# Kernel tuning notes

Measured on AMD Instinct MI355X. Metric: run time of the kernel, lower is better.

The kernel has to match this reference:

```python
import jax, jax.numpy as jnp
import numpy as np

EPS = 1e-5
MIN_NORM = 1e-15


def artanh(x):
    return jnp.arctanh(jnp.clip(x, -1.0 + EPS, 1.0 - EPS))


def expmap0(u, c):
    # Poincare ball exponential map at the origin (HGCN style)
    sqrt_c = jnp.sqrt(c)
    u_norm = jnp.maximum(jnp.linalg.norm(u, axis=-1, keepdims=True), MIN_NORM)
    return jnp.tanh(sqrt_c * u_norm) * u / (sqrt_c * u_norm)


def mobius_add(x, y, c):
    x2 = jnp.sum(x * x, axis=-1, keepdims=True)
    y2 = jnp.sum(y * y, axis=-1, keepdims=True)
    xy = jnp.sum(x * y, axis=-1, keepdims=True)
    num = (1.0 + 2.0 * c * xy + c * y2) * x + (1.0 - c * x2) * y
    den = 1.0 + 2.0 * c * xy + (c ** 2) * x2 * y2
    return num / jnp.maximum(den, MIN_NORM)


def sqdist(x, y, c):
    sqrt_c = jnp.sqrt(c)
    ma = mobius_add(-x, y, c)
    dist = (2.0 / sqrt_c) * artanh(sqrt_c * jnp.linalg.norm(ma, axis=-1))
    return dist ** 2


def setup_inputs() -> dict:
    key = jax.random.key(0)
    k1, k2 = jax.random.split(key)
    B, T, N, C, K = 8, 12, 325, 32, 100
    # scale down so points land well inside the unit ball (curvature c=1)
    node_repr = 0.05 * jax.random.normal(k1, (B, T, N, C), dtype=jnp.float32)
    centroid_weight = 0.05 * jax.random.normal(k2, (K, C), dtype=jnp.float32)
    c = jnp.ones((1,), dtype=jnp.float32)
    return {"node_repr": node_repr, "centroid_weight": centroid_weight, "c": c}


def reference(node_repr, centroid_weight, c):
    cc = c[0]
    B, T, N, C = node_repr.shape
    # centroid embedding lookup of arange(K) == the weight table itself
    centroids = expmap0(centroid_weight, cc)          # [K, C]
    x = node_repr[..., None, :]                        # [B, T, N, 1, C]
    node_centroid_dist = sqdist(x, centroids, cc)      # [B, T, N, K] via broadcast
    graph_centroid_dist = jnp.sum(node_centroid_dist, axis=1) / N  # [B, N, K] (faithful to dim=1 in source)
    return graph_centroid_dist, node_centroid_dist
```

## Files before the change

kernel.cpp:

```cpp
#include <hip/hip_runtime.h>

namespace {
constexpr int B = 8, T = 12, N = 325, C = 32, K = 100;
constexpr int KPAD = 36;
constexpr int NPB = 2;
constexpr int NPAIRS = (N + NPB - 1) / NPB;
constexpr float EPSF = 1e-5f;
constexpr float MIN_NORM = 1e-15f;
}

__global__ __launch_bounds__(256) void hcd_kernel(
    const float* __restrict__ x_g,
    const float* __restrict__ cw,
    const float* __restrict__ cptr,
    float* __restrict__ out0,
    float* __restrict__ out1)
{
  __shared__ float yl[K][KPAD];
  __shared__ float y2l[K];
  __shared__ float x2l[NPB][T];

  const int tid = threadIdx.x;
  const int b  = blockIdx.x / NPAIRS;
  const int np = blockIdx.x % NPAIRS;
  const int n0 = np * NPB;
  const float c  = cptr[0];
  const float sc = sqrtf(c);
  const float inv_c4 = 4.f / c;
  const float HLN2 = 0.34657359028f;
  const float TLOG2E = 2.88539008178f;

  if (tid < K) {
    float u[C];
    float u2 = 0.f;
    #pragma unroll
    for (int q = 0; q < C / 4; ++q) {
      float4 v = *(const float4*)(cw + tid * C + 4 * q);
      u[4*q+0] = v.x; u[4*q+1] = v.y; u[4*q+2] = v.z; u[4*q+3] = v.w;
    }
    #pragma unroll
    for (int i = 0; i < C; ++i) u2 = fmaf(u[i], u[i], u2);
    float z = sc * fmaxf(sqrtf(u2), MIN_NORM);
    float E  = exp2f(z * TLOG2E);
    float th = (E - 1.f) * __builtin_amdgcn_rcpf(E + 1.f);
    float f  = th * __builtin_amdgcn_rcpf(z);
    #pragma unroll
    for (int q = 0; q < C / 4; ++q) {
      float4 v = make_float4(f*u[4*q+0], f*u[4*q+1], f*u[4*q+2], f*u[4*q+3]);
      *(float4*)&yl[tid][4 * q] = v;
    }
    y2l[tid] = f * f * u2;
  }

  if (tid >= 128 && tid < 128 + NPB * T) {
    int i  = tid - 128;
    int nl = i / T, t = i - nl * T;
    int n  = n0 + nl;
    if (n < N) {
      const float* xr = x_g + ((size_t)(b * T + t) * N + n) * C;
      float s = 0.f;
      #pragma unroll
      for (int q = 0; q < C / 4; ++q) {
        float4 v = *(const float4*)(xr + 4 * q);
        s = fmaf(v.x, v.x, s); s = fmaf(v.y, v.y, s);
        s = fmaf(v.z, v.z, s); s = fmaf(v.w, v.w, s);
      }
      x2l[nl][t] = s;
    }
  }
  __syncthreads();

  const int grp = tid >> 7;
  const int k   = tid & 127;
  const int n   = n0 + grp;
  if (n < N) {
    const int kc = (k < K) ? k : (K - 1);

    float yk[C];
    #pragma unroll
    for (int q = 0; q < C / 4; ++q) {
      float4 v = *(const float4*)&yl[kc][4 * q];
      yk[4*q+0] = v.x; yk[4*q+1] = v.y; yk[4*q+2] = v.z; yk[4*q+3] = v.w;
    }
    const float y2 = y2l[kc];
    const float c2 = c * c;
    const float tc = 2.f * c;

    int rowbase = ((b * T) * N + n) * C;
    rowbase = __builtin_amdgcn_readfirstlane(rowbase);

    float ssum = 0.f;
    #pragma unroll
    for (int t = 0; t < T; ++t) {
      const float* xr = x_g + rowbase + t * (N * C);
      float a0 = 0.f, a1 = 0.f, a2 = 0.f, a3 = 0.f;
      #pragma unroll
      for (int j = 0; j < C; j += 4) {
        a0 = fmaf(xr[j+0], yk[j+0], a0);
        a1 = fmaf(xr[j+1], yk[j+1], a1);
        a2 = fmaf(xr[j+2], yk[j+2], a2);
        a3 = fmaf(xr[j+3], yk[j+3], a3);
      }
      const float dot = (a0 + a1) + (a2 + a3);

      const float x2 = x2l[grp][t];
      const float xy = -dot;
      const float A  = fmaf(tc, xy, 1.f) + c * y2;
      const float Bc = 1.f - c * x2;
      float num2 = A * A * x2 + Bc * Bc * y2 + 2.f * A * Bc * xy;
      num2 = fmaxf(num2, 0.f);
      float den = fmaf(c2 * x2, y2, fmaf(tc, xy, 1.f));
      den = fmaxf(den, MIN_NORM);
      float s_ = sc * __builtin_amdgcn_sqrtf(num2);
      s_ = fminf(s_, (1.f - EPSF) * den);
      float r  = (den + s_) * __builtin_amdgcn_rcpf(den - s_);
      float at = HLN2 * __builtin_amdgcn_logf(r);
      float d2 = inv_c4 * at * at;
      ssum += d2;
      if (k < K)
        out1[(((size_t)(b * T + t)) * N + n) * K + k] = d2;
    }
    if (k < K)
      out0[((size_t)b * N + n) * K + k] = ssum * (1.f / (float)N);
  }
}

extern "C" void kernel_launch(void* const* d_in, const int* in_sizes, int n_in,
                              void* d_out, int out_size, void* d_ws, size_t ws_size,
                              hipStream_t stream) {
  const void* xp = nullptr; const void* cwp = nullptr; const void* cp = nullptr;
  for (int i = 0; i < n_in; ++i) {
    if (in_sizes[i] == B * T * N * C)      xp  = d_in[i];
    else if (in_sizes[i] == K * C)         cwp = d_in[i];
    else if (in_sizes[i] == 1)             cp  = d_in[i];
  }
  if (!xp)  xp  = d_in[0];
  if (!cwp) cwp = d_in[1];
  if (!cp)  cp  = d_in[n_in - 1];

  float* out0 = (float*)d_out;
  float* out1 = out0 + (size_t)B * N * K;

  hipLaunchKernelGGL(hcd_kernel, dim3(B * NPAIRS), dim3(256), 0, stream,
                     (const float*)xp, (const float*)cwp, (const float*)cp,
                     out0, out1);
}
```

Baseline: 18.65 us.

## Use 5 nodes per block, per-thread centroid expmap, scalar-load x rows

Each block now handles 5 nodes with 640 threads (two waves per node) instead of 2 nodes with 256 threads, which cuts the number of blocks. The shared-memory centroid table is removed: each thread loads its centroid row from global memory and recomputes the expmap scaling itself. The per-timestep x row is read through inline-asm s_load_dwordx16 scalar loads with an explicit wait, replacing the compiler's per-element loads. In exchange, the expmap work is repeated across waves, each load waits fully before compute so there is no overlap, and the x2 setup no longer bounds-checks n, which relies on N being divisible by 5.

```diff
diff --git a/kernel.cpp b/kernel.cpp
--- a/kernel.cpp
+++ b/kernel.cpp
@@ -2,22 +2,21 @@
 
 namespace {
 constexpr int B = 8, T = 12, N = 325, C = 32, K = 100;
-constexpr int KPAD = 36;
-constexpr int NPB = 2;
-constexpr int NPAIRS = (N + NPB - 1) / NPB;
+constexpr int NPB = 5;
+constexpr int NPAIRS = N / NPB;
 constexpr float EPSF = 1e-5f;
 constexpr float MIN_NORM = 1e-15f;
 }
 
-__global__ __launch_bounds__(256) void hcd_kernel(
+typedef float f32x16 __attribute__((ext_vector_type(16)));
+
+__global__ __launch_bounds__(640) void hcd_kernel(
     const float* __restrict__ x_g,
     const float* __restrict__ cw,
     const float* __restrict__ cptr,
     float* __restrict__ out0,
     float* __restrict__ out1)
 {
-  __shared__ float yl[K][KPAD];
-  __shared__ float y2l[K];
   __shared__ float x2l[NPB][T];
 
   const int tid = threadIdx.x;
@@ -30,99 +29,105 @@
   const float HLN2 = 0.34657359028f;
   const float TLOG2E = 2.88539008178f;
 
-  if (tid < K) {
-    float u[C];
+  if (tid < NPB * T) {
+    int nl_ = tid / T, t = tid - nl_ * T;
+    const float* xr = x_g + ((size_t)(b * T + t) * N + (n0 + nl_)) * C;
+    float s = 0.f;
+    #pragma unroll
+    for (int q = 0; q < C / 4; ++q) {
+      float4 v = *(const float4*)(xr + 4 * q);
+      s = fmaf(v.x, v.x, s); s = fmaf(v.y, v.y, s);
+      s = fmaf(v.z, v.z, s); s = fmaf(v.w, v.w, s);
+    }
+    x2l[nl_][t] = s;
+  }
+
+  const int wave = tid >> 6;
+  const int lane = tid & 63;
+  const int nl = wave >> 1;
+  const int h  = wave & 1;
+  const int k  = h * 64 + lane;
+  const int kc = (k < K) ? k : K - 1;
+  const bool pred = (k < K);
+
+  float yk[C];
+  float y2;
+  {
+    const float* yr = cw + kc * C;
+    #pragma unroll
+    for (int q = 0; q < C / 4; ++q) {
+      float4 v = *(const float4*)(yr + 4 * q);
+      yk[4*q+0] = v.x; yk[4*q+1] = v.y; yk[4*q+2] = v.z; yk[4*q+3] = v.w;
+    }
     float u2 = 0.f;
     #pragma unroll
-    for (int q = 0; q < C / 4; ++q) {
-      float4 v = *(const float4*)(cw + tid * C + 4 * q);
-      u[4*q+0] = v.x; u[4*q+1] = v.y; u[4*q+2] = v.z; u[4*q+3] = v.w;
-    }
-    #pragma unroll
-    for (int i = 0; i < C; ++i) u2 = fmaf(u[i], u[i], u2);
+    for (int i = 0; i < C; ++i) u2 = fmaf(yk[i], yk[i], u2);
     float z = sc * fmaxf(sqrtf(u2), MIN_NORM);
     float E  = exp2f(z * TLOG2E);
     float th = (E - 1.f) * __builtin_amdgcn_rcpf(E + 1.f);
     float f  = th * __builtin_amdgcn_rcpf(z);
     #pragma unroll
-    for (int q = 0; q < C / 4; ++q) {
-      float4 v = make_float4(f*u[4*q+0], f*u[4*q+1], f*u[4*q+2], f*u[4*q+3]);
-      *(float4*)&yl[tid][4 * q] = v;
-    }
-    y2l[tid] = f * f * u2;
-  }
-
-  if (tid >= 128 && tid < 128 + NPB * T) {
-    int i  = tid - 128;
-    int nl = i / T, t = i - nl * T;
-    int n  = n0 + nl;
-    if (n < N) {
-      const float* xr = x_g + ((size_t)(b * T + t) * N + n) * C;
-      float s = 0.f;
-      #pragma unroll
-      for (int q = 0; q < C / 4; ++q) {
-        float4 v = *(const float4*)(xr + 4 * q);
-        s = fmaf(v.x, v.x, s); s = fmaf(v.y, v.y, s);
-        s = fmaf(v.z, v.z, s); s = fmaf(v.w, v.w, s);
-      }
-      x2l[nl][t] = s;
-    }
+    for (int i = 0; i < C; ++i) yk[i] *= f;
+    y2 = f * f * u2;
   }
   __syncthreads();
 
-  const int grp = tid >> 7;
-  const int k   = tid & 127;
-  const int n   = n0 + grp;
-  if (n < N) {
-    const int kc = (k < K) ? k : (K - 1);
+  const int n = n0 + nl;
+  int rowbase = ((b * T) * N + n) * C;
+  rowbase = __builtin_amdgcn_readfirstlane(rowbase);
+  const float* xbase = x_g + rowbase;
 
-    float yk[C];
+  const float c2 = c * c;
+  const float tc = 2.f * c;
+  float ssum = 0.f;
+
+  #pragma unroll
+  for (int t = 0; t < T; ++t) {
+    const float* xt = xbase + t * (N * C);
+    f32x16 xa, xv;
+    asm volatile(
+        "s_load_dwordx16 %0, %2, 0x0\n\t"
+        "s_load_dwordx16 %1, %2, 0x40\n\t"
+        "s_waitcnt lgkmcnt(0)"
+        : "=&s"(xa), "=&s"(xv)
+        : "s"(xt));
+
+    float a0 = 0.f, a1 = 0.f, a2 = 0.f, a3 = 0.f;
     #pragma unroll
-    for (int q = 0; q < C / 4; ++q) {
-      float4 v = *(const float4*)&yl[kc][4 * q];
-      yk[4*q+0] = v.x; yk[4*q+1] = v.y; yk[4*q+2] = v.z; yk[4*q+3] = v.w;
+    for (int i = 0; i < 16; i += 4) {
+      a0 = fmaf(xa[i+0], yk[i+0], a0);
+      a1 = fmaf(xa[i+1], yk[i+1], a1);
+      a2 = fmaf(xa[i+2], yk[i+2], a2);
+      a3 = fmaf(xa[i+3], yk[i+3], a3);
     }
-    const float y2 = y2l[kc];
-    const float c2 = c * c;
-    const float tc = 2.f * c;
+    #pragma unroll
+    for (int i = 0; i < 16; i += 4) {
+      a0 = fmaf(xv[i+0], yk[16+i+0], a0);
+      a1 = fmaf(xv[i+1], yk[16+i+1], a1);
+      a2 = fmaf(xv[i+2], yk[16+i+2], a2);
+      a3 = fmaf(xv[i+3], yk[16+i+3], a3);
+    }
+    const float dot = (a0 + a1) + (a2 + a3);
 
-    int rowbase = ((b * T) * N + n) * C;
-    rowbase = __builtin_amdgcn_readfirstlane(rowbase);
-
-    float ssum = 0.f;
-    #pragma unroll
-    for (int t = 0; t < T; ++t) {
-      const float* xr = x_g + rowbase + t * (N * C);
-      float a0 = 0.f, a1 = 0.f, a2 = 0.f, a3 = 0.f;
-      #pragma unroll
-      for (int j = 0; j < C; j += 4) {
-        a0 = fmaf(xr[j+0], yk[j+0], a0);
-        a1 = fmaf(xr[j+1], yk[j+1], a1);
-        a2 = fmaf(xr[j+2], yk[j+2], a2);
-        a3 = fmaf(xr[j+3], yk[j+3], a3);
-      }
-      const float dot = (a0 + a1) + (a2 + a3);
-
-      const float x2 = x2l[grp][t];
-      const float xy = -dot;
-      const float A  = fmaf(tc, xy, 1.f) + c * y2;
-      const float Bc = 1.f - c * x2;
-      float num2 = A * A * x2 + Bc * Bc * y2 + 2.f * A * Bc * xy;
-      num2 = fmaxf(num2, 0.f);
-      float den = fmaf(c2 * x2, y2, fmaf(tc, xy, 1.f));
-      den = fmaxf(den, MIN_NORM);
-      float s_ = sc * __builtin_amdgcn_sqrtf(num2);
-      s_ = fminf(s_, (1.f - EPSF) * den);
-      float r  = (den + s_) * __builtin_amdgcn_rcpf(den - s_);
-      float at = HLN2 * __builtin_amdgcn_logf(r);
-      float d2 = inv_c4 * at * at;
-      ssum += d2;
-      if (k < K)
-        out1[(((size_t)(b * T + t)) * N + n) * K + k] = d2;
-    }
-    if (k < K)
-      out0[((size_t)b * N + n) * K + k] = ssum * (1.f / (float)N);
+    const float x2 = x2l[nl][t];
+    const float xy = -dot;
+    const float A  = fmaf(tc, xy, 1.f) + c * y2;
+    const float Bc = 1.f - c * x2;
+    float num2 = A * A * x2 + Bc * Bc * y2 + 2.f * A * Bc * xy;
+    num2 = fmaxf(num2, 0.f);
+    float den = fmaf(c2 * x2, y2, fmaf(tc, xy, 1.f));
+    den = fmaxf(den, MIN_NORM);
+    float s_ = sc * __builtin_amdgcn_sqrtf(num2);
+    s_ = fminf(s_, (1.f - EPSF) * den);
+    float r  = (den + s_) * __builtin_amdgcn_rcpf(den - s_);
+    float at = HLN2 * __builtin_amdgcn_logf(r);
+    float d2 = inv_c4 * at * at;
+    ssum += d2;
+    if (pred)
+      out1[(((size_t)(b * T + t)) * N + n) * K + k] = d2;
   }
+  if (pred)
+    out0[((size_t)b * N + n) * K + k] = ssum * (1.f / (float)N);
 }
 
 extern "C" void kernel_launch(void* const* d_in, const int* in_sizes, int n_in,
@@ -141,7 +146,7 @@
   float* out0 = (float*)d_out;
   float* out1 = out0 + (size_t)B * N * K;
 
-  hipLaunchKernelGGL(hcd_kernel, dim3(B * NPAIRS), dim3(256), 0, stream,
+  hipLaunchKernelGGL(hcd_kernel, dim3(B * NPAIRS), dim3(640), 0, stream,
                      (const float*)xp, (const float*)cwp, (const float*)cp,
                      out0, out1);
 }
```

Result: slower. 22.35 us (+19.9%).

## Compute node-centroid dot products with split-bf16 MFMA, five nodes per block

Applied to the files above, without the earlier changes.

Replaces the scalar per-thread 32-element FMA dot products with MFMA 16x16x32 bf16 instructions. Each fp32 operand is split into a high and a low bf16 part and three MFMAs are issued to keep close to fp32 accuracy. Each block now processes five nodes, one wave per node, with time steps mapped to MFMA rows and centroids to columns. The graph sum is reduced with cross-lane shuffles. This cuts VALU work and redundant global reads of x, at the cost of padding waste (T=12 padded to 16, K=100 padded to 112) and a small precision loss from dropping the low×low term.

```diff
diff --git a/kernel.cpp b/kernel.cpp
--- a/kernel.cpp
+++ b/kernel.cpp
@@ -2,22 +2,36 @@
 
 namespace {
 constexpr int B = 8, T = 12, N = 325, C = 32, K = 100;
-constexpr int KPAD = 36;
-constexpr int NPB = 2;
-constexpr int NPAIRS = (N + NPB - 1) / NPB;
+constexpr int NPB = 5;
+constexpr int NPAIRS = N / NPB;
+constexpr int KT = 7;
+constexpr int KP = KT * 16;
 constexpr float EPSF = 1e-5f;
 constexpr float MIN_NORM = 1e-15f;
 }
 
-__global__ __launch_bounds__(256) void hcd_kernel(
+typedef __attribute__((ext_vector_type(8))) short bf16x8;
+typedef __attribute__((ext_vector_type(4))) float f32x4;
+
+__device__ __forceinline__ unsigned short bf16_rne(float x) {
+  unsigned int u = __float_as_uint(x);
+  unsigned int r = u + 0x7FFFu + ((u >> 16) & 1u);
+  return (unsigned short)(r >> 16);
+}
+__device__ __forceinline__ float bf16_f(unsigned short h) {
+  return __uint_as_float(((unsigned int)h) << 16);
+}
+
+__global__ __launch_bounds__(320) void hcd_kernel(
     const float* __restrict__ x_g,
     const float* __restrict__ cw,
     const float* __restrict__ cptr,
     float* __restrict__ out0,
     float* __restrict__ out1)
 {
-  __shared__ float yl[K][KPAD];
-  __shared__ float y2l[K];
+  __shared__ unsigned short yh[KP][C];
+  __shared__ unsigned short ylo[KP][C];
+  __shared__ float y2l[KP];
   __shared__ float x2l[NPB][T];
 
   const int tid = threadIdx.x;
@@ -30,80 +44,111 @@
   const float HLN2 = 0.34657359028f;
   const float TLOG2E = 2.88539008178f;
 
-  if (tid < K) {
-    float u[C];
-    float u2 = 0.f;
-    #pragma unroll
-    for (int q = 0; q < C / 4; ++q) {
-      float4 v = *(const float4*)(cw + tid * C + 4 * q);
-      u[4*q+0] = v.x; u[4*q+1] = v.y; u[4*q+2] = v.z; u[4*q+3] = v.w;
+  if (tid < KP) {
+    float y[C];
+    float y2 = 0.f;
+    if (tid < K) {
+      float u2 = 0.f;
+      #pragma unroll
+      for (int q = 0; q < C / 4; ++q) {
+        float4 v = *(const float4*)(cw + tid * C + 4 * q);
+        y[4*q+0] = v.x; y[4*q+1] = v.y; y[4*q+2] = v.z; y[4*q+3] = v.w;
+      }
+      #pragma unroll
+      for (int i = 0; i < C; ++i) u2 = fmaf(y[i], y[i], u2);
+      float z = sc * fmaxf(sqrtf(u2), MIN_NORM);
+      float E  = exp2f(z * TLOG2E);
+      float th = (E - 1.f) * __builtin_amdgcn_rcpf(E + 1.f);
+      float f  = th * __builtin_amdgcn_rcpf(z);
+      #pragma unroll
+      for (int i = 0; i < C; ++i) y[i] *= f;
+      y2 = f * f * u2;
+    } else {
+      #pragma unroll
+      for (int i = 0; i < C; ++i) y[i] = 0.f;
     }
     #pragma unroll
-    for (int i = 0; i < C; ++i) u2 = fmaf(u[i], u[i], u2);
-    float z = sc * fmaxf(sqrtf(u2), MIN_NORM);
-    float E  = exp2f(z * TLOG2E);
-    float th = (E - 1.f) * __builtin_amdgcn_rcpf(E + 1.f);
-    float f  = th * __builtin_amdgcn_rcpf(z);
-    #pragma unroll
-    for (int q = 0; q < C / 4; ++q) {
-      float4 v = make_float4(f*u[4*q+0], f*u[4*q+1], f*u[4*q+2], f*u[4*q+3]);
-      *(float4*)&yl[tid][4 * q] = v;
+    for (int i = 0; i < C; ++i) {
+      unsigned short h = bf16_rne(y[i]);
+      yh[tid][i]  = h;
+      ylo[tid][i] = bf16_rne(y[i] - bf16_f(h));
     }
-    y2l[tid] = f * f * u2;
+    y2l[tid] = y2;
   }
 
   if (tid >= 128 && tid < 128 + NPB * T) {
     int i  = tid - 128;
     int nl = i / T, t = i - nl * T;
-    int n  = n0 + nl;
-    if (n < N) {
-      const float* xr = x_g + ((size_t)(b * T + t) * N + n) * C;
-      float s = 0.f;
-      #pragma unroll
-      for (int q = 0; q < C / 4; ++q) {
-        float4 v = *(const float4*)(xr + 4 * q);
-        s = fmaf(v.x, v.x, s); s = fmaf(v.y, v.y, s);
-        s = fmaf(v.z, v.z, s); s = fmaf(v.w, v.w, s);
-      }
-      x2l[nl][t] = s;
+    const float* xr = x_g + ((size_t)(b * T + t) * N + (n0 + nl)) * C;
+    float s = 0.f;
+    #pragma unroll
+    for (int q = 0; q < C / 4; ++q) {
+      float4 v = *(const float4*)(xr + 4 * q);
+      s = fmaf(v.x, v.x, s); s = fmaf(v.y, v.y, s);
+      s = fmaf(v.z, v.z, s); s = fmaf(v.w, v.w, s);
     }
+    x2l[nl][t] = s;
+  }
+
+  const int wave = tid >> 6;
+  const int lane = tid & 63;
+  const int l16  = lane & 15;
+  const int g    = lane >> 4;
+  const int n    = n0 + wave;
+
+  const int trow = (l16 < T) ? l16 : 0;
+  const float* xrow = x_g + (((size_t)(b * T + trow) * N + n) * C) + 8 * g;
+  float4 v0 = *(const float4*)(xrow);
+  float4 v1 = *(const float4*)(xrow + 4);
+  if (l16 >= T) { v0 = make_float4(0,0,0,0); v1 = make_float4(0,0,0,0); }
+  float xe[8] = {v0.x, v0.y, v0.z, v0.w, v1.x, v1.y, v1.z, v1.w};
+  bf16x8 ah, al;
+  #pragma unroll
+  for (int i = 0; i < 8; ++i) {
+    unsigned short h = bf16_rne(xe[i]);
+    ah[i] = (short)h;
+    al[i] = (short)bf16_rne(xe[i] - bf16_f(h));
   }
   __syncthreads();
 
-  const int grp = tid >> 7;
-  const int k   = tid & 127;
-  const int n   = n0 + grp;
-  if (n < N) {
-    const int kc = (k < K) ? k : (K - 1);
+  bf16x8 bh[KT], bl[KT];
+  #pragma unroll
+  for (int kt = 0; kt < KT; ++kt) {
+    bh[kt] = *(const bf16x8*)&yh [16 * kt + l16][8 * g];
+    bl[kt] = *(const bf16x8*)&ylo[16 * kt + l16][8 * g];
+  }
 
-    float yk[C];
+  f32x4 acc[KT];
+  #pragma unroll
+  for (int kt = 0; kt < KT; ++kt) {
+    f32x4 a = {0.f, 0.f, 0.f, 0.f};
+    a = __builtin_amdgcn_mfma_f32_16x16x32_bf16(al, bh[kt], a, 0, 0, 0);
+    a = __builtin_amdgcn_mfma_f32_16x16x32_bf16(ah, bl[kt], a, 0, 0, 0);
+    a = __builtin_amdgcn_mfma_f32_16x16x32_bf16(ah, bh[kt], a, 0, 0, 0);
+    acc[kt] = a;
+  }
+
+  const float c2 = c * c;
+  const float tc = 2.f * c;
+  float x2r[4];
+  #pragma unroll
+  for (int reg = 0; reg < 4; ++reg) {
+    int t = 4 * g + reg;
+    x2r[reg] = x2l[wave][(t < T) ? t : 0];
+  }
+
+  #pragma unroll
+  for (int kt = 0; kt < KT; ++kt) {
+    const int k = 16 * kt + l16;
+    const bool kv = (k < K);
+    const float y2 = y2l[16 * kt + l16];
+    float ps = 0.f;
     #pragma unroll
-    for (int q = 0; q < C / 4; ++q) {
-      float4 v = *(const float4*)&yl[kc][4 * q];
-      yk[4*q+0] = v.x; yk[4*q+1] = v.y; yk[4*q+2] = v.z; yk[4*q+3] = v.w;
-    }
-    const float y2 = y2l[kc];
-    const float c2 = c * c;
-    const float tc = 2.f * c;
-
-    int rowbase = ((b * T) * N + n) * C;
-    rowbase = __builtin_amdgcn_readfirstlane(rowbase);
-
-    float ssum = 0.f;
-    #pragma unroll
-    for (int t = 0; t < T; ++t) {
-      const float* xr = x_g + rowbase + t * (N * C);
-      float a0 = 0.f, a1 = 0.f, a2 = 0.f, a3 = 0.f;
-      #pragma unroll
-      for (int j = 0; j < C; j += 4) {
-        a0 = fmaf(xr[j+0], yk[j+0], a0);
-        a1 = fmaf(xr[j+1], yk[j+1], a1);
-        a2 = fmaf(xr[j+2], yk[j+2], a2);
-        a3 = fmaf(xr[j+3], yk[j+3], a3);
-      }
-      const float dot = (a0 + a1) + (a2 + a3);
-
-      const float x2 = x2l[grp][t];
+    for (int reg = 0; reg < 4; ++reg) {
+      const int t = 4 * g + reg;
+      const bool tv = (t < T);
+      const float dot = acc[kt][reg];
+      const float x2 = x2r[reg];
       const float xy = -dot;
       const float A  = fmaf(tc, xy, 1.f) + c * y2;
       const float Bc = 1.f - c * x2;
@@ -116,12 +161,14 @@
       float r  = (den + s_) * __builtin_amdgcn_rcpf(den - s_);
       float at = HLN2 * __builtin_amdgcn_logf(r);
       float d2 = inv_c4 * at * at;
-      ssum += d2;
-      if (k < K)
+      if (tv & kv)
         out1[(((size_t)(b * T + t)) * N + n) * K + k] = d2;
+      ps += tv ? d2 : 0.f;
     }
-    if (k < K)
-      out0[((size_t)b * N + n) * K + k] = ssum * (1.f / (float)N);
+    ps += __shfl_xor(ps, 16);
+    ps += __shfl_xor(ps, 32);
+    if (g == 0 && kv)
+      out0[((size_t)b * N + n) * K + k] = ps * (1.f / (float)N);
   }
 }
 
@@ -141,7 +188,7 @@
   float* out0 = (float*)d_out;
   float* out1 = out0 + (size_t)B * N * K;
 
-  hipLaunchKernelGGL(hcd_kernel, dim3(B * NPAIRS), dim3(256), 0, stream,
+  hipLaunchKernelGGL(hcd_kernel, dim3(B * NPAIRS), dim3(320), 0, stream,
                      (const float*)xp, (const float*)cwp, (const float*)cp,
                      out0, out1);
 }
```

Result: faster. 17.69 us (-5.1%).
